# Performance work log

Hardware: AMD Instinct MI355X
Metric: run time of the kernel (lower is better)

The kernel has to match this reference:

```python
import jax, jax.numpy as jnp
import numpy as np

N, E, F, H, C1 = 50000, 1_600_000, 48, 1, 16  # nodes, edges, in_feats, heads, conv out


def setup_inputs() -> dict:
    key = jax.random.key(0)
    ks = jax.random.split(key, 12)
    in_ = jax.random.normal(ks[0], (N, F), dtype=jnp.float32)
    edge_index = jax.random.randint(ks[1], (2, E), 0, N, dtype=jnp.int64)
    labels = jax.random.bernoulli(ks[2], 0.5, (N, 1)).astype(jnp.float32)
    weights = jax.random.uniform(ks[3], (N, 1), dtype=jnp.float32) + 0.5
    s = 0.1  # PyG FeaStConv init: normal(0, 0.1)
    W = jax.random.normal(ks[4], (F, H * C1), dtype=jnp.float32) * s
    u = jax.random.normal(ks[5], (F, H), dtype=jnp.float32) * s
    c = jax.random.normal(ks[6], (H,), dtype=jnp.float32) * s
    bias = jax.random.normal(ks[7], (C1,), dtype=jnp.float32) * s
    lin1_w = jax.random.normal(ks[8], (C1, 8), dtype=jnp.float32) * (1.0 / np.sqrt(C1))
    lin1_b = jnp.zeros((8,), dtype=jnp.float32)
    out_w = jax.random.normal(ks[9], (8, 1), dtype=jnp.float32) * (1.0 / np.sqrt(8))
    out_b = jnp.zeros((1,), dtype=jnp.float32)
    return {"in_": in_, "edge_index": edge_index, "labels": labels,
            "weights": weights, "W": W, "u": u, "c": c, "bias": bias,
            "lin1_w": lin1_w, "lin1_b": lin1_b, "out_w": out_w, "out_b": out_b}


def feast_conv(x, edge_index, W, u, c, bias):
    n = x.shape[0]
    loop = jnp.arange(n, dtype=edge_index.dtype)  # add_self_loops=True
    src = jnp.concatenate([edge_index[0], loop])
    dst = jnp.concatenate([edge_index[1], loop])
    xj = x[src]                                   # [E+N, F] gather
    xi = x[dst]
    q = jax.nn.softmax((xj - xi) @ u + c, axis=-1)            # [E+N, H]
    xw = (xj @ W).reshape(-1, H, C1)                           # [E+N, H, C1]
    msg = jnp.einsum('ehc,eh->ec', xw, q)                      # [E+N, C1]
    agg = jax.ops.segment_sum(msg, dst, num_segments=n)        # scatter-sum
    deg = jax.ops.segment_sum(jnp.ones_like(dst, dtype=x.dtype), dst, num_segments=n)
    return agg / jnp.maximum(deg, 1.0)[:, None] + bias         # mean aggregation


def reference(in_, edge_index, labels, weights, W, u, c, bias, lin1_w, lin1_b, out_w, out_b):
    x = jax.nn.relu(feast_conv(in_, edge_index, W, u, c, bias))
    x = jax.nn.relu(x @ lin1_w + lin1_b)
    p = jax.nn.sigmoid(x @ out_w + out_b)                      # [N, 1]
    eps = 1e-7
    pc = jnp.clip(p, eps, 1.0 - eps)
    bce = -(labels * jnp.log(pc) + (1.0 - labels) * jnp.log(1.0 - pc))
    loss = jnp.mean(weights * bce)
    return (loss, p)
```

## Files before the change

### kernel.cpp

```cpp
#include <hip/hip_runtime.h>

constexpr int N_NODES  = 50000;
constexpr int N_EDGES  = 1600000;
constexpr int F_IN     = 48;
constexpr int C1_OUT   = 16;

constexpr int BNODES    = 64;
constexpr int NBINS     = 782;
constexpr int FILL_BLKS = 256;
constexpr int EPB       = N_EDGES / FILL_BLKS;
constexpr int SCAP      = 16;
constexpr int OCAP      = 16384;
constexpr int BIN_INTS  = FILL_BLKS * SCAP;
constexpr int ROWCAP    = 96;
constexpr int XW_BLKS   = 49;

constexpr size_t OCNT_OFF  = 0;
constexpr size_t OFLOW_OFF = 256;
constexpr size_t PART_OFF  = OFLOW_OFF + (size_t)OCAP * 4;
constexpr size_t XW_OFF    = PART_OFF + 4096;
constexpr size_t GSLOT_OFF = XW_OFF + (size_t)N_NODES * C1_OUT * 4;

__device__ __forceinline__ void xw_body(int n, const float* __restrict__ x,
                                        const float* __restrict__ W,
                                        float* __restrict__ xw)
{
    const float4* xr = (const float4*)(x + (long)n * F_IN);
    float h[C1_OUT];
    #pragma unroll
    for (int c = 0; c < C1_OUT; ++c) h[c] = 0.f;
    #pragma unroll
    for (int k = 0; k < F_IN / 4; ++k) {
        float4 v = xr[k];
        #pragma unroll
        for (int c = 0; c < C1_OUT; ++c) {
            h[c] = fmaf(v.x, W[(4*k+0)*C1_OUT + c],
                   fmaf(v.y, W[(4*k+1)*C1_OUT + c],
                   fmaf(v.z, W[(4*k+2)*C1_OUT + c],
                   fmaf(v.w, W[(4*k+3)*C1_OUT + c], h[c]))));
        }
    }
    float4* o = (float4*)(xw + (long)n * C1_OUT);
    o[0] = make_float4(h[0],  h[1],  h[2],  h[3]);
    o[1] = make_float4(h[4],  h[5],  h[6],  h[7]);
    o[2] = make_float4(h[8],  h[9],  h[10], h[11]);
    o[3] = make_float4(h[12], h[13], h[14], h[15]);
}

__global__ __launch_bounds__(1024)
void k_fill_xw(const int* __restrict__ src, const int* __restrict__ dst,
               int* __restrict__ gslot, int* __restrict__ ocnt,
               unsigned int* __restrict__ oflow,
               const float* __restrict__ x, const float* __restrict__ W,
               float* __restrict__ xw)
{
    __shared__ int lcnt[NBINS];
    __shared__ int lstage[NBINS * SCAP];

    if (blockIdx.x >= FILL_BLKS) {
        int n = (blockIdx.x - FILL_BLKS) * 1024 + threadIdx.x;
        if (n < N_NODES) xw_body(n, x, W, xw);
        return;
    }

    int tid = threadIdx.x;
    if (tid < NBINS) lcnt[tid] = 0;
    __syncthreads();

    int e0 = blockIdx.x * EPB;
    for (int i = tid; i < EPB; i += 1024) {
        int e = e0 + i;
        int s = src[e], d = dst[e];
        int b = d >> 6;
        int p = atomicAdd(&lcnt[b], 1);
        if (p < SCAP) {
            lstage[(b << 4) + p] = (s << 6) | (d & 63);
        } else {
            int g = atomicAdd(ocnt, 1);
            if (g < OCAP) oflow[g] = ((unsigned)s << 16) | (unsigned)d;
        }
    }
    __syncthreads();

    for (int idx = tid; idx < NBINS * SCAP; idx += 1024) {
        int b = idx >> 4, s = idx & 15;
        int v = (s < lcnt[b]) ? lstage[idx] : -1;
        gslot[((size_t)b * FILL_BLKS + blockIdx.x) * SCAP + s] = v;
    }
}

__device__ __forceinline__ float node_epilogue(
    float4 a, int n, float inv, const float* __restrict__ xw,
    const float* __restrict__ bias, const float* __restrict__ lin1_w,
    const float* __restrict__ lin1_b, const float* __restrict__ out_w,
    const float* __restrict__ out_b, const float* __restrict__ labels,
    const float* __restrict__ weights, float* __restrict__ out,
    float* s16, int lane)
{
    if (lane < 4) {
        float4 v  = ((const float4*)(xw + (size_t)n * C1_OUT))[lane];
        float4 b4 = ((const float4*)bias)[lane];
        float4 h;
        h.x = fmaxf(fmaf(a.x + v.x, inv, b4.x), 0.f);
        h.y = fmaxf(fmaf(a.y + v.y, inv, b4.y), 0.f);
        h.z = fmaxf(fmaf(a.z + v.z, inv, b4.z), 0.f);
        h.w = fmaxf(fmaf(a.w + v.w, inv, b4.w), 0.f);
        ((float4*)s16)[lane] = h;
    }
    float x2 = 0.f;
    if (lane < 8) {
        x2 = lin1_b[lane];
        #pragma unroll
        for (int k = 0; k < C1_OUT; ++k)
            x2 = fmaf(s16[k], lin1_w[k * 8 + lane], x2);
        x2 = fmaxf(x2, 0.f) * out_w[lane];
    }
    x2 += __shfl_xor(x2, 1, 64);
    x2 += __shfl_xor(x2, 2, 64);
    x2 += __shfl_xor(x2, 4, 64);
    float ret = 0.f;
    if (lane == 0) {
        float z = x2 + out_b[0];
        float p = 1.f / (1.f + __expf(-z));
        out[1 + n] = p;
        const float eps = 1e-7f;
        float pc = fminf(fmaxf(p, eps), 1.f - eps);
        float y  = labels[n];
        ret = weights[n] * (-(y * __logf(pc) + (1.f - y) * __logf(1.f - pc)));
    }
    return ret;
}

__global__ __launch_bounds__(256)
void k_agg(const int* __restrict__ gslot, const int* __restrict__ ocnt,
           const unsigned int* __restrict__ oflow, const float* __restrict__ xw,
           const float* __restrict__ bias, const float* __restrict__ lin1_w,
           const float* __restrict__ lin1_b, const float* __restrict__ out_w,
           const float* __restrict__ out_b, const float* __restrict__ labels,
           const float* __restrict__ weights, float* __restrict__ out,
           float* __restrict__ partials)
{
    __shared__ int ndeg[BNODES];
    __shared__ unsigned short lrow[BNODES][ROWCAP];
    __shared__ float s16[4][16];
    __shared__ float sLossW[4];

    int B = blockIdx.x, tid = threadIdx.x, lane = tid & 63, w = tid >> 6;

    if (tid < BNODES) ndeg[tid] = 0;
    __syncthreads();

    const int4* sp = (const int4*)(gslot + (size_t)B * BIN_INTS);
    #pragma unroll
    for (int k = 0; k < 4; ++k) {
        int4 q = sp[tid + (k << 8)];
        #define SC1(v) if ((v) >= 0) { int ln = (v) & 63;               \
            int p = atomicAdd(&ndeg[ln], 1);                            \
            if (p < ROWCAP) lrow[ln][p] = (unsigned short)((unsigned)(v) >> 6); }
        SC1(q.x); SC1(q.y); SC1(q.z); SC1(q.w);
        #undef SC1
    }
    int oc = *ocnt; if (oc > OCAP) oc = OCAP;
    for (int i = tid; i < oc; i += 256) {
        unsigned v = oflow[i];
        int d = (int)(v & 0xffffu);
        if ((d >> 6) == B) {
            int ln = d & 63;
            int p = atomicAdd(&ndeg[ln], 1);
            if (p < ROWCAP) lrow[ln][p] = (unsigned short)(v >> 16);
        }
    }
    __syncthreads();

    int rslot = lane >> 2, c4 = lane & 3;
    float lossw = 0.f;
    for (int i = 0; i < 16; ++i) {
        int ln = w * 16 + i;
        int n = B * BNODES + ln;
        if (n >= N_NODES) break;
        int deg = ndeg[ln];
        if (deg > ROWCAP) deg = ROWCAP;
        float4 a = make_float4(0.f, 0.f, 0.f, 0.f);
        for (int j0 = 0; j0 < deg; j0 += 16) {
            int j = j0 + rslot;
            if (j < deg) {
                int s = lrow[ln][j];
                float4 v = ((const float4*)(xw + (size_t)s * C1_OUT))[c4];
                a.x += v.x; a.y += v.y; a.z += v.z; a.w += v.w;
            }
        }
        #pragma unroll
        for (int off = 4; off < 64; off <<= 1) {
            a.x += __shfl_xor(a.x, off, 64);
            a.y += __shfl_xor(a.y, off, 64);
            a.z += __shfl_xor(a.z, off, 64);
            a.w += __shfl_xor(a.w, off, 64);
        }
        lossw += node_epilogue(a, n, 1.f / (float)(deg + 1), xw, bias, lin1_w,
                               lin1_b, out_w, out_b, labels, weights, out,
                               s16[w], lane);
    }
    if (lane == 0) sLossW[w] = lossw;
    __syncthreads();
    if (tid == 0)
        partials[B] = sLossW[0] + sLossW[1] + sLossW[2] + sLossW[3];
}

__global__ __launch_bounds__(1024)
void k_loss_final(const float* __restrict__ partials, float* __restrict__ out)
{
    __shared__ float sw[16];
    int tid = threadIdx.x, lane = tid & 63, wv = tid >> 6;
    float s = (tid < NBINS) ? partials[tid] : 0.f;
    #pragma unroll
    for (int off = 32; off > 0; off >>= 1) s += __shfl_down(s, off, 64);
    if (lane == 0) sw[wv] = s;
    __syncthreads();
    if (tid == 0) {
        float t = 0.f;
        #pragma unroll
        for (int k = 0; k < 16; ++k) t += sw[k];
        out[0] = t / (float)N_NODES;
    }
}

extern "C" void kernel_launch(void* const* d_in, const int* in_sizes, int n_in,
                              void* d_out, int out_size, void* d_ws, size_t ws_size,
                              hipStream_t stream)
{
    const float* x       = (const float*)d_in[0];
    const int*   eidx    = (const int*)  d_in[1];
    const float* labels  = (const float*)d_in[2];
    const float* weights = (const float*)d_in[3];
    const float* W       = (const float*)d_in[4];
    const float* bias    = (const float*)d_in[7];
    const float* lin1_w  = (const float*)d_in[8];
    const float* lin1_b  = (const float*)d_in[9];
    const float* out_w   = (const float*)d_in[10];
    const float* out_b   = (const float*)d_in[11];
    float* out = (float*)d_out;

    const int* src = eidx;
    const int* dst = eidx + N_EDGES;
    char* ws = (char*)d_ws;

    int*          ocnt     = (int*)(ws + OCNT_OFF);
    unsigned int* oflow    = (unsigned int*)(ws + OFLOW_OFF);
    float*        partials = (float*)(ws + PART_OFF);
    float*        xw       = (float*)(ws + XW_OFF);
    int*          gslot    = (int*)(ws + GSLOT_OFF);

    hipMemsetAsync(ocnt, 0, sizeof(int), stream);
    k_fill_xw<<<FILL_BLKS + XW_BLKS, 1024, 0, stream>>>(
        src, dst, gslot, ocnt, oflow, x, W, xw);
    k_agg<<<NBINS, 256, 0, stream>>>(
        gslot, ocnt, oflow, xw, bias, lin1_w, lin1_b,
        out_w, out_b, labels, weights, out, partials);
    k_loss_final<<<1, 1024, 0, stream>>>(partials, out);
}
```

Baseline: 168.0 us.

## Interleave two nodes per wave in aggregation and batch epilogue across lanes

The aggregation loop now handles two destination nodes per iteration, so each wave has two independent gather streams in flight. The per-node sums go into a shared accumulator. The MLP/sigmoid/BCE epilogue then runs once, with 16 lanes each handling one node, instead of a serialized per-node epilogue using only a few lanes. All int4 bin loads are also issued before the shared-memory scatter to overlap load latency, and ROWCAP grows slightly. The aim is more memory-level parallelism and less serialized epilogue work, at the cost of extra registers and LDS. Nodes beyond N_NODES in the last block are no longer early-exited during aggregation.

```diff
diff --git a/kernel.cpp b/kernel.cpp
--- a/kernel.cpp
+++ b/kernel.cpp
@@ -12,7 +12,7 @@
 constexpr int SCAP      = 16;
 constexpr int OCAP      = 16384;
 constexpr int BIN_INTS  = FILL_BLKS * SCAP;
-constexpr int ROWCAP    = 96;
+constexpr int ROWCAP    = 98;
 constexpr int XW_BLKS   = 49;
 
 constexpr size_t OCNT_OFF  = 0;
@@ -89,48 +89,6 @@
     }
 }
 
-__device__ __forceinline__ float node_epilogue(
-    float4 a, int n, float inv, const float* __restrict__ xw,
-    const float* __restrict__ bias, const float* __restrict__ lin1_w,
-    const float* __restrict__ lin1_b, const float* __restrict__ out_w,
-    const float* __restrict__ out_b, const float* __restrict__ labels,
-    const float* __restrict__ weights, float* __restrict__ out,
-    float* s16, int lane)
-{
-    if (lane < 4) {
-        float4 v  = ((const float4*)(xw + (size_t)n * C1_OUT))[lane];
-        float4 b4 = ((const float4*)bias)[lane];
-        float4 h;
-        h.x = fmaxf(fmaf(a.x + v.x, inv, b4.x), 0.f);
-        h.y = fmaxf(fmaf(a.y + v.y, inv, b4.y), 0.f);
-        h.z = fmaxf(fmaf(a.z + v.z, inv, b4.z), 0.f);
-        h.w = fmaxf(fmaf(a.w + v.w, inv, b4.w), 0.f);
-        ((float4*)s16)[lane] = h;
-    }
-    float x2 = 0.f;
-    if (lane < 8) {
-        x2 = lin1_b[lane];
-        #pragma unroll
-        for (int k = 0; k < C1_OUT; ++k)
-            x2 = fmaf(s16[k], lin1_w[k * 8 + lane], x2);
-        x2 = fmaxf(x2, 0.f) * out_w[lane];
-    }
-    x2 += __shfl_xor(x2, 1, 64);
-    x2 += __shfl_xor(x2, 2, 64);
-    x2 += __shfl_xor(x2, 4, 64);
-    float ret = 0.f;
-    if (lane == 0) {
-        float z = x2 + out_b[0];
-        float p = 1.f / (1.f + __expf(-z));
-        out[1 + n] = p;
-        const float eps = 1e-7f;
-        float pc = fminf(fmaxf(p, eps), 1.f - eps);
-        float y  = labels[n];
-        ret = weights[n] * (-(y * __logf(pc) + (1.f - y) * __logf(1.f - pc)));
-    }
-    return ret;
-}
-
 __global__ __launch_bounds__(256)
 void k_agg(const int* __restrict__ gslot, const int* __restrict__ ocnt,
            const unsigned int* __restrict__ oflow, const float* __restrict__ xw,
@@ -142,7 +100,7 @@
 {
     __shared__ int ndeg[BNODES];
     __shared__ unsigned short lrow[BNODES][ROWCAP];
-    __shared__ float s16[4][16];
+    __shared__ float acc[BNODES][17];
     __shared__ float sLossW[4];
 
     int B = blockIdx.x, tid = threadIdx.x, lane = tid & 63, w = tid >> 6;
@@ -151,16 +109,18 @@
     __syncthreads();
 
     const int4* sp = (const int4*)(gslot + (size_t)B * BIN_INTS);
-    #pragma unroll
-    for (int k = 0; k < 4; ++k) {
-        int4 q = sp[tid + (k << 8)];
-        #define SC1(v) if ((v) >= 0) { int ln = (v) & 63;               \
-            int p = atomicAdd(&ndeg[ln], 1);                            \
-            if (p < ROWCAP) lrow[ln][p] = (unsigned short)((unsigned)(v) >> 6); }
-        SC1(q.x); SC1(q.y); SC1(q.z); SC1(q.w);
-        #undef SC1
-    }
+    int4 q0 = sp[tid], q1 = sp[tid + 256], q2 = sp[tid + 512], q3 = sp[tid + 768];
+
     int oc = *ocnt; if (oc > OCAP) oc = OCAP;
+
+    #define SC1(v) if ((v) >= 0) { int ln = (v) & 63;               \
+        int p = atomicAdd(&ndeg[ln], 1);                            \
+        if (p < ROWCAP) lrow[ln][p] = (unsigned short)((unsigned)(v) >> 6); }
+    SC1(q0.x); SC1(q0.y); SC1(q0.z); SC1(q0.w);
+    SC1(q1.x); SC1(q1.y); SC1(q1.z); SC1(q1.w);
+    SC1(q2.x); SC1(q2.y); SC1(q2.z); SC1(q2.w);
+    SC1(q3.x); SC1(q3.y); SC1(q3.z); SC1(q3.w);
+    #undef SC1
     for (int i = tid; i < oc; i += 256) {
         unsigned v = oflow[i];
         int d = (int)(v & 0xffffu);
@@ -173,33 +133,84 @@
     __syncthreads();
 
     int rslot = lane >> 2, c4 = lane & 3;
-    float lossw = 0.f;
-    for (int i = 0; i < 16; ++i) {
-        int ln = w * 16 + i;
-        int n = B * BNODES + ln;
-        if (n >= N_NODES) break;
-        int deg = ndeg[ln];
-        if (deg > ROWCAP) deg = ROWCAP;
-        float4 a = make_float4(0.f, 0.f, 0.f, 0.f);
-        for (int j0 = 0; j0 < deg; j0 += 16) {
+    #pragma unroll
+    for (int i = 0; i < 16; i += 2) {
+        int ln0 = w * 16 + i, ln1 = ln0 + 1;
+        int d0 = ndeg[ln0]; if (d0 > ROWCAP) d0 = ROWCAP;
+        int d1 = ndeg[ln1]; if (d1 > ROWCAP) d1 = ROWCAP;
+        int m = (d0 > d1) ? d0 : d1;
+        float4 a0 = make_float4(0.f, 0.f, 0.f, 0.f);
+        float4 a1 = make_float4(0.f, 0.f, 0.f, 0.f);
+        for (int j0 = 0; j0 < m; j0 += 16) {
             int j = j0 + rslot;
-            if (j < deg) {
-                int s = lrow[ln][j];
+            if (j < d0) {
+                int s = lrow[ln0][j];
                 float4 v = ((const float4*)(xw + (size_t)s * C1_OUT))[c4];
-                a.x += v.x; a.y += v.y; a.z += v.z; a.w += v.w;
+                a0.x += v.x; a0.y += v.y; a0.z += v.z; a0.w += v.w;
+            }
+            if (j < d1) {
+                int s = lrow[ln1][j];
+                float4 v = ((const float4*)(xw + (size_t)s * C1_OUT))[c4];
+                a1.x += v.x; a1.y += v.y; a1.z += v.z; a1.w += v.w;
             }
         }
         #pragma unroll
         for (int off = 4; off < 64; off <<= 1) {
-            a.x += __shfl_xor(a.x, off, 64);
-            a.y += __shfl_xor(a.y, off, 64);
-            a.z += __shfl_xor(a.z, off, 64);
-            a.w += __shfl_xor(a.w, off, 64);
-        }
-        lossw += node_epilogue(a, n, 1.f / (float)(deg + 1), xw, bias, lin1_w,
-                               lin1_b, out_w, out_b, labels, weights, out,
-                               s16[w], lane);
-    }
+            a0.x += __shfl_xor(a0.x, off, 64);
+            a1.x += __shfl_xor(a1.x, off, 64);
+            a0.y += __shfl_xor(a0.y, off, 64);
+            a1.y += __shfl_xor(a1.y, off, 64);
+            a0.z += __shfl_xor(a0.z, off, 64);
+            a1.z += __shfl_xor(a1.z, off, 64);
+            a0.w += __shfl_xor(a0.w, off, 64);
+            a1.w += __shfl_xor(a1.w, off, 64);
+        }
+        if (lane < 8) {
+            int ln = (lane < 4) ? ln0 : ln1;
+            float4 a = (lane < 4) ? a0 : a1;
+            int c = lane & 3;
+            acc[ln][c * 4 + 0] = a.x;
+            acc[ln][c * 4 + 1] = a.y;
+            acc[ln][c * 4 + 2] = a.z;
+            acc[ln][c * 4 + 3] = a.w;
+        }
+    }
+
+    float lossw = 0.f;
+    if (lane < 16) {
+        int ln = w * 16 + lane;
+        int n = B * BNODES + ln;
+        if (n < N_NODES) {
+            int dg = ndeg[ln]; if (dg > ROWCAP) dg = ROWCAP;
+            float inv = 1.f / (float)(dg + 1);
+            const float4* xs4 = (const float4*)(xw + (size_t)n * C1_OUT);
+            float xs[16];
+            ((float4*)xs)[0] = xs4[0]; ((float4*)xs)[1] = xs4[1];
+            ((float4*)xs)[2] = xs4[2]; ((float4*)xs)[3] = xs4[3];
+            float h[16];
+            #pragma unroll
+            for (int c = 0; c < 16; ++c)
+                h[c] = fmaxf(fmaf(acc[ln][c] + xs[c], inv, bias[c]), 0.f);
+            float z = out_b[0];
+            #pragma unroll
+            for (int j = 0; j < 8; ++j) {
+                float t = lin1_b[j];
+                #pragma unroll
+                for (int k = 0; k < 16; ++k) t = fmaf(h[k], lin1_w[k * 8 + j], t);
+                z = fmaf(fmaxf(t, 0.f), out_w[j], z);
+            }
+            float p = 1.f / (1.f + __expf(-z));
+            out[1 + n] = p;
+            const float eps = 1e-7f;
+            float pc = fminf(fmaxf(p, eps), 1.f - eps);
+            float y  = labels[n];
+            lossw = weights[n] * (-(y * __logf(pc) + (1.f - y) * __logf(1.f - pc)));
+        }
+    }
+    lossw += __shfl_xor(lossw, 1, 64);
+    lossw += __shfl_xor(lossw, 2, 64);
+    lossw += __shfl_xor(lossw, 4, 64);
+    lossw += __shfl_xor(lossw, 8, 64);
     if (lane == 0) sLossW[w] = lossw;
     __syncthreads();
     if (tid == 0)
```

New measurement: 138.1 us. 17.8% less time.
